# Optimization experiments

Measured on AMD Instinct MI355X. Metric: run time of the kernel, lower is better.

The kernel has to match this reference:

```python
import jax, jax.numpy as jnp
import numpy as np

N = 20000      # nodes
E = 320000     # edges
B = 128        # graphs in batch
DIN = 64       # in_channels == out_channels (residual)
DEDGE = 64     # edge_attr_dim
DINS = 64      # ins_dim
H = 2          # heads
C = 64         # out_channels per head
L = 2          # num_ins (conv layers)
SLOPE = 0.2    # leaky relu negative slope
EPS = 1e-5     # batchnorm eps


def setup_inputs() -> dict:
    key = jax.random.key(0)
    ks = jax.random.split(key, 12)
    s = 0.05  # small glorot-ish init scale
    return {
        "x": jax.random.normal(ks[0], (N, DIN), jnp.float32),
        "edge_index": jax.random.randint(ks[1], (2, E), 0, N),
        "edge_attr": jax.random.normal(ks[2], (E, DEDGE), jnp.float32),
        "instr_vectors": jax.random.normal(ks[3], (L, B, DINS), jnp.float32),
        "batch": jnp.sort(jax.random.randint(ks[4], (N,), 0, B)),
        "W_l": jax.random.normal(ks[5], (L, DIN + DINS, H * C), jnp.float32) * s,
        "W_e": jax.random.normal(ks[6], (L, DEDGE + DINS, H * C), jnp.float32) * s,
        "att_l": jax.random.normal(ks[7], (L, H, C), jnp.float32) * s,
        "att_r": jax.random.normal(ks[8], (L, H, C), jnp.float32) * s,
        "att_e": jax.random.normal(ks[9], (L, H, C), jnp.float32) * s,
        "bias": jnp.zeros((L, C), jnp.float32),
        "bn_gamma": jnp.ones((L - 1, C), jnp.float32),
        "bn_beta": jnp.zeros((L - 1, C), jnp.float32),
    }


def reference(x, edge_index, edge_attr, instr_vectors, batch,
              W_l, W_e, att_l, att_r, att_e, bias, bn_gamma, bn_beta):
    src, dst = edge_index[0], edge_index[1]  # j -> i (source_to_target)
    h = x
    for i in range(L):
        ins = instr_vectors[i]                                   # [B, DINS]
        x_cat = jnp.concatenate([h, ins[batch]], axis=-1)        # [N, DIN+DINS]
        e_cat = jnp.concatenate([edge_attr, ins[batch[src]]], axis=-1)  # [E, ...]
        xl = (x_cat @ W_l[i]).reshape(-1, H, C)                  # [N,H,C] (lin_l == lin_r)
        al = (xl * att_l[i]).sum(-1)                             # [N,H]
        ar = (xl * att_r[i]).sum(-1)                             # [N,H]
        eh = (e_cat @ W_e[i]).reshape(-1, H, C)                  # [E,H,C]
        ae = (eh * att_e[i]).sum(-1)                             # [E,H]
        a = al[src] + ar[dst] + ae                               # [E,H]
        a = jnp.where(a > 0, a, SLOPE * a)                       # leaky relu
        # segment softmax over incoming edges of each target node
        m = jax.ops.segment_max(a, dst, num_segments=N)          # [N,H]
        ex = jnp.exp(a - m[dst])
        ssum = jax.ops.segment_sum(ex, dst, num_segments=N)
        alpha = ex / (ssum[dst] + 1e-16)                         # [E,H]
        out = jax.ops.segment_sum(xl[src] * alpha[:, :, None], dst, num_segments=N)
        out = out.mean(axis=1) + bias[i]                         # concat=False -> head mean
        h = out + h                                              # residual
        if i != L - 1:
            mu = h.mean(axis=0)
            var = ((h - mu) ** 2).mean(axis=0)                   # biased var (BN training)
            h = (h - mu) / jnp.sqrt(var + EPS) * bn_gamma[i] + bn_beta[i]
            h = jax.nn.relu(h)
    return h
```

## Files before the change

### kernel.cpp

```cpp
#include <hip/hip_runtime.h>
#include <hip/hip_fp16.h>
#include <math.h>

#define NN 20000
#define NE 320000
#define NB 128
#define SLOPE 0.2f
#define BN_EPS 1e-5f
#define NBLK 79

__device__ __forceinline__ unsigned short f2bf(float f) {
    unsigned int u = __float_as_uint(f);
    unsigned int r = (u + 0x7FFFu + ((u >> 16) & 1u)) >> 16;
    return (unsigned short)r;
}
__device__ __forceinline__ float bf2f(unsigned short h) {
    return __uint_as_float(((unsigned int)h) << 16);
}

__global__ __launch_bounds__(256) void k_hist(const int* __restrict__ dst, int* __restrict__ deg) {
    int e = blockIdx.x * 256 + threadIdx.x;
    if (e < NE) atomicAdd(&deg[dst[e]], 1);
}

__global__ __launch_bounds__(256) void k_scanA(const int* __restrict__ deg, int* __restrict__ bsum) {
    __shared__ int wsum[4];
    int t = threadIdx.x;
    int idx = blockIdx.x * 256 + t;
    int v = (idx < NN) ? deg[idx] : 0;
    for (int off = 32; off > 0; off >>= 1) v += __shfl_xor(v, off);
    if ((t & 63) == 0) wsum[t >> 6] = v;
    __syncthreads();
    if (t == 0) bsum[blockIdx.x] = wsum[0] + wsum[1] + wsum[2] + wsum[3];
}

__global__ __launch_bounds__(64) void k_scanB(const int* __restrict__ bsum, int* __restrict__ boff,
                                              int* __restrict__ rowptr) {
    int l = threadIdx.x;
    int v0 = (l < NBLK) ? bsum[l] : 0;
    int v1 = (64 + l < NBLK) ? bsum[64 + l] : 0;
    int o0 = v0, o1 = v1;
    for (int off = 1; off < 64; off <<= 1) { int u = __shfl_up(v0, off); if (l >= off) v0 += u; }
    int tot0 = __shfl(v0, 63);
    for (int off = 1; off < 64; off <<= 1) { int u = __shfl_up(v1, off); if (l >= off) v1 += u; }
    int tot1 = __shfl(v1, 63);
    if (l < NBLK) boff[l] = v0 - o0;
    if (64 + l < NBLK) boff[64 + l] = tot0 + v1 - o1;
    if (l == 0) rowptr[NN] = tot0 + tot1;
}

__global__ __launch_bounds__(256) void k_scanC(const int* __restrict__ deg, const int* __restrict__ boff,
                                               int* __restrict__ rowptr, int* __restrict__ cursor) {
    __shared__ int wsum[4];
    int t = threadIdx.x, lane = t & 63, w = t >> 6;
    int idx = blockIdx.x * 256 + t;
    int v = (idx < NN) ? deg[idx] : 0;
    int incl = v;
    for (int off = 1; off < 64; off <<= 1) { int u = __shfl_up(incl, off); if (lane >= off) incl += u; }
    if (lane == 63) wsum[w] = incl;
    __syncthreads();
    int pre = 0;
    for (int i = 0; i < w; ++i) pre += wsum[i];
    int excl = incl - v + pre + boff[blockIdx.x];
    if (idx < NN) { rowptr[idx] = excl; cursor[idx] = excl; }
}

__global__ __launch_bounds__(256) void k_p1(const float* __restrict__ We, const float* __restrict__ atte,
                                            float* __restrict__ ve01, float* __restrict__ w2e01) {
    int L = blockIdx.x;
    const float* WeL = We + (size_t)L * 128 * 128;
    const float* aeL = atte + L * 128;
    int t = threadIdx.x;
    int h = (t >> 6) & 1;
    int k = t & 63;
    int row = (t < 128) ? k : (64 + k);
    float acc = 0.f;
    for (int c = 0; c < 64; ++c) acc += WeL[row * 128 + h * 64 + c] * aeL[h * 64 + c];
    if (t < 128) ve01[L * 128 + t] = acc;
    else        w2e01[L * 128 + (t - 128)] = acc;
}

__global__ __launch_bounds__(256) void k_p2both(const float* __restrict__ instr, const float* __restrict__ Wl,
                                                const float* __restrict__ w2e01,
                                                float* __restrict__ insl01, float* __restrict__ ce01) {
    int blk = blockIdx.x, t = threadIdx.x;
    if (blk < 128) {
        int L = blk >> 6;
        int idx = (blk & 63) * 256 + t;
        int b = idx >> 7, j = idx & 127;
        const float* ins = instr + (size_t)L * NB * 64;
        const float* WlL = Wl + (size_t)L * 128 * 128;
        float acc = 0.f;
        for (int k = 0; k < 64; ++k) acc += ins[b * 64 + k] * WlL[(64 + k) * 128 + j];
        insl01[(size_t)L * 16384 + idx] = acc;
    } else {
        int L = blk - 128;
        int b = t >> 1, h = t & 1;
        const float* ins = instr + (size_t)L * NB * 64;
        const float* w2 = w2e01 + L * 128 + h * 64;
        float acc = 0.f;
        for (int k = 0; k < 64; ++k) acc += ins[b * 64 + k] * w2[k];
        ce01[L * 256 + b * 2 + h] = acc;
    }
}

__global__ __launch_bounds__(256) void k_node(const float* __restrict__ hcur, const float* __restrict__ Wl,
                                              const float* __restrict__ insl, const int* __restrict__ batch,
                                              const float* __restrict__ attl, const float* __restrict__ attr_,
                                              const float2* __restrict__ ce2,
                                              const float* __restrict__ scsh, int use_bn,
                                              unsigned short* __restrict__ xlh,
                                              float* __restrict__ alc, float* __restrict__ ar) {
    __shared__ float sh[8 * 64];
    int t = threadIdx.x;
    int row0 = blockIdx.x * 8;
    for (int idx = t; idx < 512; idx += 256) {
        int r = idx >> 6, k = idx & 63;
        int n = row0 + r;
        float hv = (n < NN) ? hcur[n * 64 + k] : 0.f;
        if (use_bn) hv = fmaxf(hv * scsh[k] + scsh[64 + k], 0.f);
        sh[idx] = hv;
    }
    __syncthreads();
    int w = t >> 6, lane = t & 63;
    int h = w & 1;
    int rbase = (w >> 1) * 4;
    int j = h * 64 + lane;
    float attlv = attl[j];
    float attrv = attr_[j];
    float acc0 = 0.f, acc1 = 0.f, acc2 = 0.f, acc3 = 0.f;
    for (int k = 0; k < 64; ++k) {
        float wv = Wl[k * 128 + j];
        acc0 += sh[(rbase + 0) * 64 + k] * wv;
        acc1 += sh[(rbase + 1) * 64 + k] * wv;
        acc2 += sh[(rbase + 2) * 64 + k] * wv;
        acc3 += sh[(rbase + 3) * 64 + k] * wv;
    }
    float accs[4] = {acc0, acc1, acc2, acc3};
    for (int rr = 0; rr < 4; ++rr) {
        int n = row0 + rbase + rr;
        if (n >= NN) break;
        int b = batch[n];
        float v = accs[rr] + insl[b * 128 + j];
        xlh[(size_t)n * 128 + j] = f2bf(v);
        float pl = v * attlv, pr = v * attrv;
        for (int off = 32; off > 0; off >>= 1) {
            pl += __shfl_xor(pl, off);
            pr += __shfl_xor(pr, off);
        }
        if (lane == 0) {
            float2 cb = ce2[b];
            alc[n * 2 + h] = pl + (h ? cb.y : cb.x);
            ar[n * 2 + h] = pr;
        }
    }
}

__global__ __launch_bounds__(256) void k_sced(const int* __restrict__ src, const int* __restrict__ dst,
                                              const float* __restrict__ eattr, const float* __restrict__ ve01,
                                              int* __restrict__ cursor,
                                              const float2* __restrict__ alc2, const float2* __restrict__ ar2,
                                              int2* __restrict__ csr_sd, float2* __restrict__ ae2,
                                              int2* __restrict__ rec0) {
    __shared__ float sv[256];
    int t = threadIdx.x;
    sv[t] = ve01[t];
    __syncthreads();
    int w = t >> 6, lane = t & 63;
    int l16 = lane & 15, sub = lane >> 4;
    int ebase = blockIdx.x * 256 + w * 64;
    const float4* sv4 = (const float4*)sv;
    float4 v0 = sv4[l16];
    float4 v1 = sv4[16 + l16];
    float4 v2 = sv4[32 + l16];
    float4 v3 = sv4[48 + l16];
    for (int it = 0; it < 16; ++it) {
        int e = ebase + it * 4 + sub;
        float4 f = ((const float4*)eattr)[(size_t)e * 16 + l16];
        float d00 = f.x * v0.x + f.y * v0.y + f.z * v0.z + f.w * v0.w;
        float d01 = f.x * v1.x + f.y * v1.y + f.z * v1.z + f.w * v1.w;
        float d10 = f.x * v2.x + f.y * v2.y + f.z * v2.z + f.w * v2.w;
        float d11 = f.x * v3.x + f.y * v3.y + f.z * v3.z + f.w * v3.w;
#pragma unroll
        for (int off = 1; off < 16; off <<= 1) {
            d00 += __shfl_xor(d00, off);
            d01 += __shfl_xor(d01, off);
            d10 += __shfl_xor(d10, off);
            d11 += __shfl_xor(d11, off);
        }
        if (l16 == 0) {
            int s = src[e], dd = dst[e];
            int pos = atomicAdd(&cursor[dd], 1);
            csr_sd[pos] = make_int2(s, dd);
            ae2[pos] = make_float2(d10, d11);
            float2 a_l = alc2[s];
            float2 a_r = ar2[dd];
            float a0 = a_l.x + a_r.x + d00;
            float a1 = a_l.y + a_r.y + d01;
            a0 = (a0 > 0.f) ? a0 : SLOPE * a0;
            a1 = (a1 > 0.f) ? a1 : SLOPE * a1;
            __half2 hx = __floats2half2_rn(__expf(a0), __expf(a1));
            rec0[pos] = make_int2(s, *(int*)&hx);
        }
    }
}

__global__ __launch_bounds__(256) void k_attnexp(const int2* __restrict__ csr_sd, const float2* __restrict__ ae2,
                                                 const float2* __restrict__ alc2, const float2* __restrict__ ar2,
                                                 int2* __restrict__ rec) {
    int p = blockIdx.x * 256 + threadIdx.x;
    if (p >= NE) return;
    int2 sd = csr_sd[p];
    float2 ae = ae2[p];
    float2 a_l = alc2[sd.x];
    float2 a_r = ar2[sd.y];
    float a0 = a_l.x + a_r.x + ae.x;
    float a1 = a_l.y + a_r.y + ae.y;
    a0 = (a0 > 0.f) ? a0 : SLOPE * a0;
    a1 = (a1 > 0.f) ? a1 : SLOPE * a1;
    __half2 hx = __floats2half2_rn(__expf(a0), __expf(a1));
    rec[p] = make_int2(sd.x, *(int*)&hx);
}

__global__ __launch_bounds__(256) void k_gather(const int* __restrict__ rowptr, const int2* __restrict__ rec,
                                                const unsigned int* __restrict__ xl32,
                                                const float* __restrict__ bias, const float* __restrict__ hprev,
                                                const float* __restrict__ scsh, int use_bn,
                                                float* __restrict__ hnew) {
    int t = threadIdx.x;
    int w = t >> 6, lane = t & 63;
    int n = blockIdx.x * 4 + w;
    if (n >= NN) return;
    int r0 = rowptr[n], r1 = rowptr[n + 1];
    float acc0 = 0.f, acc1 = 0.f, ss = 0.f;
    const unsigned int* xlp = xl32 + lane;
#pragma unroll 8
    for (int p = r0; p < r1; ++p) {
        int2 r = rec[p];
        __half2 hx = *(__half2*)&r.y;
        float2 e2 = __half22float2(hx);
        float ex = (lane < 32) ? e2.x : e2.y;
        unsigned int pr = xlp[(size_t)r.x * 64];
        ss += ex;
        acc0 += ex * bf2f((unsigned short)(pr & 0xFFFFu));
        acc1 += ex * bf2f((unsigned short)(pr >> 16));
    }
    float inv = 1.f / (ss + 1e-16f);
    acc0 *= inv; acc1 *= inv;
    float o0 = 0.5f * (acc0 + __shfl_xor(acc0, 32));
    float o1 = 0.5f * (acc1 + __shfl_xor(acc1, 32));
    if (lane < 32) {
        float2 hv = ((const float2*)(hprev + (size_t)n * 64))[lane];
        if (use_bn) {
            float2 sc = ((const float2*)scsh)[lane];
            float2 sf = ((const float2*)(scsh + 64))[lane];
            hv.x = fmaxf(hv.x * sc.x + sf.x, 0.f);
            hv.y = fmaxf(hv.y * sc.y + sf.y, 0.f);
        }
        float2 bv = ((const float2*)bias)[lane];
        float2 o;
        o.x = o0 + bv.x + hv.x;
        o.y = o1 + bv.y + hv.y;
        ((float2*)(hnew + (size_t)n * 64))[lane] = o;
    }
}

__global__ __launch_bounds__(256) void k_bnstat(const float* __restrict__ hbuf,
                                                float* __restrict__ part, float* __restrict__ partsq) {
    __shared__ float sA[256], sB[256];
    int t = threadIdx.x;
    int c = t & 63, r = t >> 6;
    int n0 = blockIdx.x * 80;
    float s = 0.f, s2 = 0.f;
    for (int i = 0; i < 20; ++i) {
        float v = hbuf[(size_t)(n0 + i * 4 + r) * 64 + c];
        s += v; s2 += v * v;
    }
    sA[t] = s; sB[t] = s2;
    __syncthreads();
    if (t < 64) {
        part[blockIdx.x * 64 + t]   = sA[t] + sA[t + 64] + sA[t + 128] + sA[t + 192];
        partsq[blockIdx.x * 64 + t] = sB[t] + sB[t + 64] + sB[t + 128] + sB[t + 192];
    }
}

__global__ __launch_bounds__(256) void k_bnred(const float* __restrict__ part, const float* __restrict__ partsq,
                                               const float* __restrict__ gamma, const float* __restrict__ beta,
                                               float* __restrict__ scsh) {
    __shared__ float sA[256], sB[256];
    int t = threadIdx.x;
    int c = t & 63, q = t >> 6;
    float s = 0.f, s2 = 0.f;
    for (int j = q; j < 250; j += 4) { s += part[j * 64 + c]; s2 += partsq[j * 64 + c]; }
    sA[t] = s; sB[t] = s2;
    __syncthreads();
    if (t < 64) {
        float su = sA[t] + sA[t + 64] + sA[t + 128] + sA[t + 192];
        float sq = sB[t] + sB[t + 64] + sB[t + 128] + sB[t + 192];
        float mu = su * (1.f / NN);
        float var = sq * (1.f / NN) - mu * mu;
        float sc = gamma[t] * rsqrtf(var + BN_EPS);
        scsh[t] = sc;
        scsh[64 + t] = beta[t] - mu * sc;
    }
}

extern "C" void kernel_launch(void* const* d_in, const int* in_sizes, int n_in,
                              void* d_out, int out_size, void* d_ws, size_t ws_size,
                              hipStream_t stream) {
    (void)in_sizes; (void)n_in; (void)out_size; (void)ws_size;
    const float* x     = (const float*)d_in[0];
    const int*   eidx  = (const int*)d_in[1];
    const float* eattr = (const float*)d_in[2];
    const float* instr = (const float*)d_in[3];
    const int*   batch = (const int*)d_in[4];
    const float* W_l   = (const float*)d_in[5];
    const float* W_e   = (const float*)d_in[6];
    const float* att_l = (const float*)d_in[7];
    const float* att_r = (const float*)d_in[8];
    const float* att_e = (const float*)d_in[9];
    const float* bias  = (const float*)d_in[10];
    const float* bn_g  = (const float*)d_in[11];
    const float* bn_b  = (const float*)d_in[12];
    float* out = (float*)d_out;

    const int* src = eidx;
    const int* dst = eidx + NE;

    char* ws = (char*)d_ws;
    int2*   csr_sd  = (int2*)ws;       ws += (size_t)NE * 8;
    float2* ae2     = (float2*)ws;     ws += (size_t)NE * 8;
    int2*   rec     = (int2*)ws;       ws += (size_t)NE * 8;
    unsigned short* xlh = (unsigned short*)ws; ws += (size_t)NN * 128 * 2;
    int*    deg     = (int*)ws;        ws += NN * 4;
    int*    rowptr  = (int*)ws;        ws += (NN + 1) * 4 + 4;
    int*    cursor  = (int*)ws;        ws += NN * 4;
    int*    bsum    = (int*)ws;        ws += 80 * 4;
    int*    boff    = (int*)ws;        ws += 80 * 4;
    float*  alc     = (float*)ws;      ws += NN * 2 * 4;
    float*  ar      = (float*)ws;      ws += NN * 2 * 4;
    float*  insl01  = (float*)ws;      ws += 2 * 128 * 128 * 4;
    float*  ve01    = (float*)ws;      ws += 256 * 4;
    float*  w2e01   = (float*)ws;      ws += 256 * 4;
    float*  ce01    = (float*)ws;      ws += 2 * 256 * 4;
    float*  hbuf    = (float*)ws;      ws += (size_t)NN * 64 * 4;
    float*  part    = (float*)ws;      ws += 250 * 64 * 4;
    float*  partsq  = (float*)ws;      ws += 250 * 64 * 4;
    float*  scsh    = (float*)ws;      ws += 128 * 4;

    hipMemsetAsync(deg, 0, NN * 4, stream);
    k_hist<<<(NE + 255) / 256, 256, 0, stream>>>(dst, deg);
    k_scanA<<<NBLK, 256, 0, stream>>>(deg, bsum);
    k_scanB<<<1, 64, 0, stream>>>(bsum, boff, rowptr);
    k_scanC<<<NBLK, 256, 0, stream>>>(deg, boff, rowptr, cursor);

    k_p1<<<2, 256, 0, stream>>>(W_e, att_e, ve01, w2e01);
    k_p2both<<<130, 256, 0, stream>>>(instr, W_l, w2e01, insl01, ce01);

    k_node<<<(NN + 7) / 8, 256, 0, stream>>>(x, W_l, insl01, batch,
                                             att_l, att_r, (const float2*)ce01,
                                             scsh, 0, xlh, alc, ar);
    k_sced<<<NE / 256, 256, 0, stream>>>(src, dst, eattr, ve01, cursor,
                                         (const float2*)alc, (const float2*)ar,
                                         csr_sd, ae2, rec);
    k_gather<<<NN / 4, 256, 0, stream>>>(rowptr, rec, (const unsigned int*)xlh,
                                         bias, x, scsh, 0, hbuf);
    k_bnstat<<<250, 256, 0, stream>>>(hbuf, part, partsq);
    k_bnred<<<1, 256, 0, stream>>>(part, partsq, bn_g, bn_b, scsh);

    k_node<<<(NN + 7) / 8, 256, 0, stream>>>(hbuf, W_l + 128 * 128, insl01 + 16384, batch,
                                             att_l + 128, att_r + 128, (const float2*)(ce01 + 256),
                                             scsh, 1, xlh, alc, ar);
    k_attnexp<<<(NE + 255) / 256, 256, 0, stream>>>(csr_sd, ae2,
                                                    (const float2*)alc, (const float2*)ar, rec);
    k_gather<<<NN / 4, 256, 0, stream>>>(rowptr, rec, (const unsigned int*)xlh,
                                         bias + 64, hbuf, scsh, 1, out);
}
```

Before: 308.8 us.

## Store edge records in original order and gather through a CSR permutation index

A separate permutation kernel now builds a CSR-order index of original edge ids. The edge dot and attention kernels write their outputs in original edge order, so they no longer do atomic-cursor scatters. The gather kernels then read records indirectly through the index, which adds an extra dependent load and random access to the per-edge record. The aim is to take the scattered atomic writes out of the heavy edge kernel, at the cost of indirection in the gather.

```diff
diff --git a/kernel.cpp b/kernel.cpp
--- a/kernel.cpp
+++ b/kernel.cpp
@@ -63,6 +63,14 @@
     for (int i = 0; i < w; ++i) pre += wsum[i];
     int excl = incl - v + pre + boff[blockIdx.x];
     if (idx < NN) { rowptr[idx] = excl; cursor[idx] = excl; }
+}
+
+__global__ __launch_bounds__(256) void k_perm(const int* __restrict__ dst, int* __restrict__ cursor,
+                                              int* __restrict__ inv) {
+    int e = blockIdx.x * 256 + threadIdx.x;
+    if (e >= NE) return;
+    int pos = atomicAdd(&cursor[dst[e]], 1);
+    inv[pos] = e;
 }
 
 __global__ __launch_bounds__(256) void k_p1(const float* __restrict__ We, const float* __restrict__ atte,
@@ -156,12 +164,10 @@
     }
 }
 
-__global__ __launch_bounds__(256) void k_sced(const int* __restrict__ src, const int* __restrict__ dst,
+__global__ __launch_bounds__(256) void k_edot(const int* __restrict__ src, const int* __restrict__ dst,
                                               const float* __restrict__ eattr, const float* __restrict__ ve01,
-                                              int* __restrict__ cursor,
                                               const float2* __restrict__ alc2, const float2* __restrict__ ar2,
-                                              int2* __restrict__ csr_sd, float2* __restrict__ ae2,
-                                              int2* __restrict__ rec0) {
+                                              float2* __restrict__ ae2, int2* __restrict__ rec0) {
     __shared__ float sv[256];
     int t = threadIdx.x;
     sv[t] = ve01[t];
@@ -190,9 +196,7 @@
         }
         if (l16 == 0) {
             int s = src[e], dd = dst[e];
-            int pos = atomicAdd(&cursor[dd], 1);
-            csr_sd[pos] = make_int2(s, dd);
-            ae2[pos] = make_float2(d10, d11);
+            ae2[e] = make_float2(d10, d11);
             float2 a_l = alc2[s];
             float2 a_r = ar2[dd];
             float a0 = a_l.x + a_r.x + d00;
@@ -200,29 +204,31 @@
             a0 = (a0 > 0.f) ? a0 : SLOPE * a0;
             a1 = (a1 > 0.f) ? a1 : SLOPE * a1;
             __half2 hx = __floats2half2_rn(__expf(a0), __expf(a1));
-            rec0[pos] = make_int2(s, *(int*)&hx);
-        }
-    }
-}
-
-__global__ __launch_bounds__(256) void k_attnexp(const int2* __restrict__ csr_sd, const float2* __restrict__ ae2,
+            rec0[e] = make_int2(s, *(int*)&hx);
+        }
+    }
+}
+
+__global__ __launch_bounds__(256) void k_attnexp(const int* __restrict__ src, const int* __restrict__ dst,
+                                                 const float2* __restrict__ ae2,
                                                  const float2* __restrict__ alc2, const float2* __restrict__ ar2,
                                                  int2* __restrict__ rec) {
-    int p = blockIdx.x * 256 + threadIdx.x;
-    if (p >= NE) return;
-    int2 sd = csr_sd[p];
-    float2 ae = ae2[p];
-    float2 a_l = alc2[sd.x];
-    float2 a_r = ar2[sd.y];
+    int e = blockIdx.x * 256 + threadIdx.x;
+    if (e >= NE) return;
+    int s = src[e], d = dst[e];
+    float2 ae = ae2[e];
+    float2 a_l = alc2[s];
+    float2 a_r = ar2[d];
     float a0 = a_l.x + a_r.x + ae.x;
     float a1 = a_l.y + a_r.y + ae.y;
     a0 = (a0 > 0.f) ? a0 : SLOPE * a0;
     a1 = (a1 > 0.f) ? a1 : SLOPE * a1;
     __half2 hx = __floats2half2_rn(__expf(a0), __expf(a1));
-    rec[p] = make_int2(sd.x, *(int*)&hx);
-}
-
-__global__ __launch_bounds__(256) void k_gather(const int* __restrict__ rowptr, const int2* __restrict__ rec,
+    rec[e] = make_int2(s, *(int*)&hx);
+}
+
+__global__ __launch_bounds__(256) void k_gather(const int* __restrict__ rowptr, const int* __restrict__ inv,
+                                                const int2* __restrict__ rec,
                                                 const unsigned int* __restrict__ xl32,
                                                 const float* __restrict__ bias, const float* __restrict__ hprev,
                                                 const float* __restrict__ scsh, int use_bn,
@@ -236,7 +242,8 @@
     const unsigned int* xlp = xl32 + lane;
 #pragma unroll 8
     for (int p = r0; p < r1; ++p) {
-        int2 r = rec[p];
+        int e = inv[p];
+        int2 r = rec[e];
         __half2 hx = *(__half2*)&r.y;
         float2 e2 = __half22float2(hx);
         float ex = (lane < 32) ? e2.x : e2.y;
@@ -245,8 +252,8 @@
         acc0 += ex * bf2f((unsigned short)(pr & 0xFFFFu));
         acc1 += ex * bf2f((unsigned short)(pr >> 16));
     }
-    float inv = 1.f / (ss + 1e-16f);
-    acc0 *= inv; acc1 *= inv;
+    float inv_s = 1.f / (ss + 1e-16f);
+    acc0 *= inv_s; acc1 *= inv_s;
     float o0 = 0.5f * (acc0 + __shfl_xor(acc0, 32));
     float o1 = 0.5f * (acc1 + __shfl_xor(acc1, 32));
     if (lane < 32) {
@@ -328,9 +335,10 @@
     const int* dst = eidx + NE;
 
     char* ws = (char*)d_ws;
-    int2*   csr_sd  = (int2*)ws;       ws += (size_t)NE * 8;
     float2* ae2     = (float2*)ws;     ws += (size_t)NE * 8;
-    int2*   rec     = (int2*)ws;       ws += (size_t)NE * 8;
+    int2*   rec0    = (int2*)ws;       ws += (size_t)NE * 8;
+    int2*   rec1    = (int2*)ws;       ws += (size_t)NE * 8;
+    int*    inv     = (int*)ws;        ws += (size_t)NE * 4;
     unsigned short* xlh = (unsigned short*)ws; ws += (size_t)NN * 128 * 2;
     int*    deg     = (int*)ws;        ws += NN * 4;
     int*    rowptr  = (int*)ws;        ws += (NN + 1) * 4 + 4;
@@ -353,6 +361,7 @@
     k_scanA<<<NBLK, 256, 0, stream>>>(deg, bsum);
     k_scanB<<<1, 64, 0, stream>>>(bsum, boff, rowptr);
     k_scanC<<<NBLK, 256, 0, stream>>>(deg, boff, rowptr, cursor);
+    k_perm<<<(NE + 255) / 256, 256, 0, stream>>>(dst, cursor, inv);
 
     k_p1<<<2, 256, 0, stream>>>(W_e, att_e, ve01, w2e01);
     k_p2both<<<130, 256, 0, stream>>>(instr, W_l, w2e01, insl01, ce01);
@@ -360,10 +369,9 @@
     k_node<<<(NN + 7) / 8, 256, 0, stream>>>(x, W_l, insl01, batch,
                                              att_l, att_r, (const float2*)ce01,
                                              scsh, 0, xlh, alc, ar);
-    k_sced<<<NE / 256, 256, 0, stream>>>(src, dst, eattr, ve01, cursor,
-                                         (const float2*)alc, (const float2*)ar,
-                                         csr_sd, ae2, rec);
-    k_gather<<<NN / 4, 256, 0, stream>>>(rowptr, rec, (const unsigned int*)xlh,
+    k_edot<<<NE / 256, 256, 0, stream>>>(src, dst, eattr, ve01,
+                                         (const float2*)alc, (const float2*)ar, ae2, rec0);
+    k_gather<<<NN / 4, 256, 0, stream>>>(rowptr, inv, rec0, (const unsigned int*)xlh,
                                          bias, x, scsh, 0, hbuf);
     k_bnstat<<<250, 256, 0, stream>>>(hbuf, part, partsq);
     k_bnred<<<1, 256, 0, stream>>>(part, partsq, bn_g, bn_b, scsh);
@@ -371,8 +379,8 @@
     k_node<<<(NN + 7) / 8, 256, 0, stream>>>(hbuf, W_l + 128 * 128, insl01 + 16384, batch,
                                              att_l + 128, att_r + 128, (const float2*)(ce01 + 256),
                                              scsh, 1, xlh, alc, ar);
-    k_attnexp<<<(NE + 255) / 256, 256, 0, stream>>>(csr_sd, ae2,
-                                                    (const float2*)alc, (const float2*)ar, rec);
-    k_gather<<<NN / 4, 256, 0, stream>>>(rowptr, rec, (const unsigned int*)xlh,
+    k_attnexp<<<(NE + 255) / 256, 256, 0, stream>>>(src, dst, ae2,
+                                                    (const float2*)alc, (const float2*)ar, rec1);
+    k_gather<<<NN / 4, 256, 0, stream>>>(rowptr, inv, rec1, (const unsigned int*)xlh,
                                          bias + 64, hbuf, scsh, 1, out);
 }
```

Result: slower. 339.0 us (+9.8%).
